# Optimization experiments

Hardware: AMD Instinct MI355X
Metric: run time of the kernel (lower is better)

The kernel has to match this reference:

```python
import jax, jax.numpy as jnp
import numpy as np

V, E, HID, NLAYERS, NL, B, T = 21128, 512, 512, 2, 9, 64, 512
H = HID // 2  # per-direction hidden


def setup_inputs() -> dict:
    key = jax.random.key(0)
    ks = jax.random.split(key, 12)
    n = lambda k, sh, sc=0.05: (jax.random.normal(k, sh, dtype=jnp.float32) * sc)
    return {
        "input_ids": jax.random.randint(ks[0], (B, T), 0, V),
        "labels": jax.random.randint(ks[1], (B, T), 0, NL),
        "emb": n(ks[2], (V, E), 0.02),
        # stacked LSTM params: [layer, direction, ...]; layer0 input = E == HID
        "w_ih": n(ks[3], (NLAYERS, 2, 4 * H, HID)),
        "w_hh": n(ks[4], (NLAYERS, 2, 4 * H, H)),
        "b_ih": n(ks[5], (NLAYERS, 2, 4 * H)),
        "b_hh": n(ks[6], (NLAYERS, 2, 4 * H)),
        "cls_w": n(ks[7], (NL, HID)),
        "cls_b": n(ks[8], (NL,)),
        "start_trans": jax.random.uniform(ks[9], (NL,), jnp.float32, -0.1, 0.1),
        "end_trans": jax.random.uniform(ks[10], (NL,), jnp.float32, -0.1, 0.1),
        "trans": jax.random.uniform(ks[11], (NL, NL), jnp.float32, -0.1, 0.1),
    }


def _lstm_dir(x, wi, wh, bi, bh, reverse):
    # x: [B,T,I] -> h: [B,T,H]; torch gate order i,f,g,o
    xp = jnp.einsum('bti,gi->btg', x, wi) + bi + bh  # [B,T,4H]
    if reverse:
        xp = xp[:, ::-1]
    h0 = jnp.zeros((x.shape[0], wh.shape[1]), x.dtype)

    def step(carry, xt):
        h, c = carry
        g = xt + h @ wh.T
        i, f, gg, o = jnp.split(g, 4, axis=-1)
        c = jax.nn.sigmoid(f) * c + jax.nn.sigmoid(i) * jnp.tanh(gg)
        h = jax.nn.sigmoid(o) * jnp.tanh(c)
        return (h, c), h

    _, hs = jax.lax.scan(step, (h0, h0), xp.swapaxes(0, 1))
    hs = hs.swapaxes(0, 1)
    return hs[:, ::-1] if reverse else hs


def _crf_neg_llh(logits, labels, start_trans, end_trans, trans):
    # torchcrf forward, full mask, reduction='sum'; returns -sum(log-likelihood)
    em0 = logits[:, 0]  # [B,NL]
    alpha0 = start_trans[None, :] + em0
    num0 = start_trans[labels[:, 0]] + jnp.take_along_axis(em0, labels[:, 0:1], 1)[:, 0]

    def step(carry, xt):
        alpha, num, prev = carry
        em, tag = xt  # [B,NL], [B]
        alpha = jax.nn.logsumexp(alpha[:, :, None] + trans[None] + em[:, None, :], axis=1)
        num = num + trans[prev, tag] + jnp.take_along_axis(em, tag[:, None], 1)[:, 0]
        return (alpha, num, tag), None

    xs = (logits[:, 1:].swapaxes(0, 1), labels[:, 1:].swapaxes(0, 1))
    (alpha, num, last), _ = jax.lax.scan(step, (alpha0, num0, labels[:, 0]), xs)
    denom = jax.nn.logsumexp(alpha + end_trans[None, :], axis=1)
    num = num + end_trans[last]
    return -jnp.sum(num - denom)


def reference(input_ids, labels, emb, w_ih, w_hh, b_ih, b_hh, cls_w, cls_b,
              start_trans, end_trans, trans):
    x = emb[input_ids]  # [B,T,E]
    for l in range(NLAYERS):
        fwd = _lstm_dir(x, w_ih[l, 0], w_hh[l, 0], b_ih[l, 0], b_hh[l, 0], False)
        bwd = _lstm_dir(x, w_ih[l, 1], w_hh[l, 1], b_ih[l, 1], b_hh[l, 1], True)
        x = jnp.concatenate([fwd, bwd], axis=-1)  # [B,T,HID]
    logits = jnp.einsum('bth,lh->btl', x, cls_w) + cls_b  # [B,T,NL]
    return _crf_neg_llh(logits, labels, start_trans, end_trans, trans)
```

## Files before the change

### kernel.cpp

```cpp
#include <hip/hip_runtime.h>

#define B_   64
#define T_   512
#define HID_ 512
#define H_   256
#define G4   1024
#define N2   2048
#define M_   (B_*T_)
#define NL_  9

typedef short short8 __attribute__((ext_vector_type(8)));
typedef float f32x4 __attribute__((ext_vector_type(4)));
typedef _Float16 f16x2 __attribute__((ext_vector_type(2)));

__device__ inline float bf2f(unsigned short u) {
  unsigned int x = ((unsigned int)u) << 16;
  return __builtin_bit_cast(float, x);
}
__device__ inline unsigned short f2bf(float f) {
  unsigned int u = __builtin_bit_cast(unsigned int, f);
  return (unsigned short)((u + 0x7fffu + ((u >> 16) & 1u)) >> 16);
}
__device__ inline unsigned short f2h(float f) {
  _Float16 h = (_Float16)f;
  return __builtin_bit_cast(unsigned short, h);
}
__device__ inline float fdot2(unsigned int w, unsigned int h, float acc) {
#if __has_builtin(__builtin_amdgcn_fdot2)
  return __builtin_amdgcn_fdot2(__builtin_bit_cast(f16x2, w),
                                __builtin_bit_cast(f16x2, h), acc, false);
#else
  f16x2 a = __builtin_bit_cast(f16x2, w), b = __builtin_bit_cast(f16x2, h);
  return acc + (float)a[0]*(float)b[0] + (float)a[1]*(float)b[1];
#endif
}
__device__ inline float sigm(float x)     { return 1.f / (1.f + __expf(-x)); }
__device__ inline float tanhfast(float x) { return 1.f - 2.f / (__expf(2.f*x) + 1.f); }

__device__ inline float xhalf_sum(float x) {
#if __has_builtin(__builtin_amdgcn_permlane32_swap)
  typedef unsigned int u32x2 __attribute__((ext_vector_type(2)));
  u32x2 r = __builtin_amdgcn_permlane32_swap(
      __builtin_bit_cast(unsigned int, x), __builtin_bit_cast(unsigned int, x),
      false, false);
  return x + __builtin_bit_cast(float, r[1]);
#else
  return x + __shfl_xor(x, 32, 64);
#endif
}

__device__ inline void gload16(const unsigned short* g, unsigned short* l) {
  __builtin_amdgcn_global_load_lds(
      (const __attribute__((address_space(1))) void*)g,
      (__attribute__((address_space(3))) void*)l, 16, 0, 0);
}

__global__ void k_cast_bf16(const float* __restrict__ src, unsigned short* __restrict__ dst, int n) {
  int i = blockIdx.x*256 + threadIdx.x;
  if (i < n) dst[i] = f2bf(src[i]);
}

__global__ void k_pack_whh(const float* __restrict__ whh, unsigned int* __restrict__ wr,
                           unsigned int* __restrict__ wl) {
  int idx = blockIdx.x*256 + threadIdx.x;
  int q   = idx & 3;
  int t   = (idx >> 2) & 511;
  int i4  = (idx >> 11) & 63;
  int ld  = idx >> 17;
  int lane = t & 63, wave = t >> 6;
  int u  = wave*32 + (lane & 31);
  int kh = lane >> 5;
  int g, k0;
  if (i4 < 48) { g = i4/12; int j = i4%12; k0 = kh*128 + 8*j + 2*q; }
  else         { int m = i4-48; g = m>>2; int jl = m&3; k0 = kh*128 + 96 + 8*jl + 2*q; }
  int c = g*256 + u;
  const float* src = whh + ((size_t)ld*1024 + c)*256 + k0;
  unsigned int pack = (unsigned int)f2h(src[0]) | ((unsigned int)f2h(src[1]) << 16);
  if (i4 < 48) wr[(((size_t)ld*48 + i4)*512 + t)*4 + q] = pack;
  else         wl[(((size_t)ld*16 + (i4-48))*512 + t)*4 + q] = pack;
}

__global__ void k_bias_sum(const float* __restrict__ bi, const float* __restrict__ bh,
                           float* __restrict__ bs) {
  int i = blockIdx.x*256 + threadIdx.x;
  if (i < 4096) bs[i] = bi[i] + bh[i];
}

__global__ void k_cls_pad(const float* __restrict__ w, unsigned short* __restrict__ dst) {
  int i = blockIdx.x*256 + threadIdx.x;
  if (i < 16*512) {
    int n = i >> 9, k = i & 511;
    dst[i] = (n < NL_) ? f2bf(w[n*512 + k]) : (unsigned short)0;
  }
}

__global__ void k_embed(const int* __restrict__ ids, const float* __restrict__ emb,
                        unsigned short* __restrict__ x0) {
  int idx = blockIdx.x*256 + threadIdx.x;
  int m  = idx >> 7;
  int e4 = (idx & 127) << 2;
  int id = ids[m];
  float4 v = *(const float4*)(emb + (size_t)id*HID_ + e4);
  unsigned short* dst = x0 + (size_t)m*HID_ + e4;
  dst[0]=f2bf(v.x); dst[1]=f2bf(v.y); dst[2]=f2bf(v.z); dst[3]=f2bf(v.w);
}

__global__ __launch_bounds__(256) void k_gemm_inproj(const unsigned short* __restrict__ A,
    const unsigned short* __restrict__ Bt, const float* __restrict__ bias,
    unsigned short* __restrict__ C) {
  __shared__ unsigned short As[4096];
  __shared__ unsigned short Bs[4096];
  int tid  = threadIdx.x;
  int lane = tid & 63, w = tid >> 6;
  int wm = w >> 1, wn = w & 1;
  int n0 = blockIdx.x * 128;
  int m0 = blockIdx.y * 128;

  int c0 = tid, c1 = 256 + tid;
  int ar0 = c0 & 127, ak0 = c0 >> 7;
  int ar1 = c1 & 127, ak1 = c1 >> 7;
  const unsigned short* gA0 = A  + (size_t)(m0 + ar0)*512 + ak0*8;
  const unsigned short* gA1 = A  + (size_t)(m0 + ar1)*512 + ak1*8;
  const unsigned short* gB0 = Bt + (size_t)(n0 + ar0)*512 + ak0*8;
  const unsigned short* gB1 = Bt + (size_t)(n0 + ar1)*512 + ak1*8;
  unsigned short* lA0 = As + (size_t)c0*8;
  unsigned short* lA1 = As + (size_t)c1*8;
  unsigned short* lB0 = Bs + (size_t)c0*8;
  unsigned short* lB1 = Bs + (size_t)c1*8;

  int r = lane & 15, kg = lane >> 4;
  const short8* Af = (const short8*)As + (size_t)kg*128 + wm*64 + r;
  const short8* Bf = (const short8*)Bs + (size_t)kg*128 + wn*64 + r;

  f32x4 acc[4][4];
  #pragma unroll
  for (int mi = 0; mi < 4; mi++)
    #pragma unroll
    for (int ni = 0; ni < 4; ni++)
      acc[mi][ni] = (f32x4){0,0,0,0};

  #pragma unroll 1
  for (int kt = 0; kt < 16; kt++) {
    gload16(gA0, lA0); gload16(gA1, lA1);
    gload16(gB0, lB0); gload16(gB1, lB1);
    gA0 += 32; gA1 += 32; gB0 += 32; gB1 += 32;
    __syncthreads();
    short8 av[4], bv[4];
    #pragma unroll
    for (int i = 0; i < 4; i++) { av[i] = Af[i*16]; bv[i] = Bf[i*16]; }
    #pragma unroll
    for (int mi = 0; mi < 4; mi++)
      #pragma unroll
      for (int ni = 0; ni < 4; ni++)
        acc[mi][ni] = __builtin_amdgcn_mfma_f32_16x16x32_bf16(av[mi], bv[ni], acc[mi][ni], 0, 0, 0);
    __syncthreads();
  }

  int rbase = m0 + wm*64 + (lane >> 4)*4;
  int cbase = n0 + wn*64 + (lane & 15);
  #pragma unroll
  for (int ni = 0; ni < 4; ni++) {
    int n = cbase + ni*16;
    float bb = bias[n];
    int dd = n >> 10, nn = n & 1023, uu = nn & 255, gg = nn >> 8;
    size_t ncol = (size_t)dd*1024 + uu*4 + gg;
    #pragma unroll
    for (int mi = 0; mi < 4; mi++)
      #pragma unroll
      for (int rr = 0; rr < 4; rr++)
        C[(size_t)(rbase + mi*16 + rr)*N2 + ncol] = f2bf(acc[mi][ni][rr] + bb);
  }
}

__global__ __launch_bounds__(256) void k_cls(const unsigned short* __restrict__ X,
    const unsigned short* __restrict__ Wb, const float* __restrict__ cb,
    float* __restrict__ out) {
  int lane = threadIdx.x & 63, wave = threadIdx.x >> 6;
  int m0 = blockIdx.x*64 + wave*16;
  int r = lane & 15, kg = lane >> 4;
  const short8* Ap = (const short8*)(X  + (size_t)(m0 + r)*512 + kg*8);
  const short8* Bp = (const short8*)(Wb + (size_t)r*512 + kg*8);
  f32x4 acc = {0,0,0,0};
  #pragma unroll
  for (int kb = 0; kb < 16; kb++)
    acc = __builtin_amdgcn_mfma_f32_16x16x32_bf16(Ap[kb*4], Bp[kb*4], acc, 0, 0, 0);
  int row0 = m0 + (lane >> 4)*4, col = lane & 15;
  if (col < NL_) {
    float bb = cb[col];
    #pragma unroll
    for (int rr = 0; rr < 4; rr++)
      out[(size_t)(row0+rr)*NL_ + col] = acc[rr] + bb;
  }
}

#define DOT4(ACC, W0, W1, W2, W3, HH) do { \
  ACC = fdot2(W0, (HH).x, ACC); ACC = fdot2(W1, (HH).y, ACC); \
  ACC = fdot2(W2, (HH).z, ACC); ACC = fdot2(W3, (HH).w, ACC); } while(0)

__global__ __launch_bounds__(512, 2) void k_rec(const unsigned short* __restrict__ xp,
    const uint4* __restrict__ wr, const uint4* __restrict__ wl,
    unsigned short* __restrict__ xout, int layer) {
  extern __shared__ char smem[];
  unsigned int* hA = (unsigned int*)(smem + 131072);
  unsigned int* hB = hA + 128;
  int t = threadIdx.x;
  int lane = t & 63, wave = t >> 6;
  int u  = wave*32 + (lane & 31);
  int kh = lane >> 5;
  bool lo = (lane < 32);
  int b = blockIdx.x >> 1, d = blockIdx.x & 1;
  int ld = layer*2 + d;

  char* wlb = smem + (((unsigned)(t*16)) ^ (((unsigned)t & 0x38u) << 1));
  {
    const uint4* src = wl + (size_t)ld*16*512 + t;
    #pragma unroll
    for (int m = 0; m < 16; m++)
      *(uint4*)(wlb + m*8192) = src[(size_t)m*512];
  }
  uint4 wq[48];
  {
    const uint4* src = wr + (size_t)ld*48*512 + t;
    #pragma unroll
    for (int i = 0; i < 48; i++) wq[i] = src[(size_t)i*512];
  }
  if (t < 128) hA[t] = 0u;
  float cst = 0.f;
  const unsigned short* xbase = xp + (size_t)b*T_*N2 + (size_t)d*G4 + u*4;
  unsigned short* obase = xout + (size_t)b*T_*HID_ + d*H_ + u;
  __syncthreads();

  int tt = d ? (T_-1) : 0;
  ushort4 nx = {0,0,0,0};
  if (lo) nx = *(const ushort4*)(xbase + (size_t)tt*N2);
  #pragma unroll 1
  for (int step = 0; step < T_; step++) {
    const uint4* hs = (const uint4*)((step & 1) ? hB : hA) + kh*16;
    float a0 = bf2f(nx.x), a1 = bf2f(nx.y), a2 = bf2f(nx.z), a3 = bf2f(nx.w);
    int ttn = d ? (T_-2-step) : (step+1);
    if (lo && step < T_-1)
      nx = *(const ushort4*)(xbase + (size_t)ttn*N2);
    #pragma unroll
    for (int j = 0; j < 12; j++) {
      uint4 hh = hs[j];
      DOT4(a0, wq[j].x,    wq[j].y,    wq[j].z,    wq[j].w,    hh);
      DOT4(a1, wq[12+j].x, wq[12+j].y, wq[12+j].z, wq[12+j].w, hh);
      DOT4(a2, wq[24+j].x, wq[24+j].y, wq[24+j].z, wq[24+j].w, hh);
      DOT4(a3, wq[36+j].x, wq[36+j].y, wq[36+j].z, wq[36+j].w, hh);
    }
    #pragma unroll
    for (int jl = 0; jl < 4; jl++) {
      uint4 hh = hs[12 + jl];
      uint4 q0 = *(const uint4*)(wlb + (0*4+jl)*8192);
      uint4 q1 = *(const uint4*)(wlb + (1*4+jl)*8192);
      uint4 q2 = *(const uint4*)(wlb + (2*4+jl)*8192);
      uint4 q3 = *(const uint4*)(wlb + (3*4+jl)*8192);
      DOT4(a0, q0.x, q0.y, q0.z, q0.w, hh);
      DOT4(a1, q1.x, q1.y, q1.z, q1.w, hh);
      DOT4(a2, q2.x, q2.y, q2.z, q2.w, hh);
      DOT4(a3, q3.x, q3.y, q3.z, q3.w, hh);
    }
    a0 = xhalf_sum(a0); a1 = xhalf_sum(a1);
    a2 = xhalf_sum(a2); a3 = xhalf_sum(a3);
    if (lo) {
      float gi = sigm(a0);
      float gf = sigm(a1);
      float gg = tanhfast(a2);
      float go = sigm(a3);
      cst = gf*cst + gi*gg;
      float h = go * tanhfast(cst);
      _Float16* hn = (_Float16*)((step & 1) ? hA : hB);
      hn[u] = (_Float16)h;
      obase[(size_t)tt*HID_] = f2bf(h);
    }
    __syncthreads();
    tt = ttn;
  }
}

__global__ void k_zero(float* out) { if (threadIdx.x == 0) out[0] = 0.f; }

__global__ void k_crf(const float* __restrict__ logits, const int* __restrict__ labels,
                      const float* __restrict__ st, const float* __restrict__ et,
                      const float* __restrict__ tr, float* __restrict__ out) {
  int b = blockIdx.x, lane = threadIdx.x;
  bool act = lane < NL_;
  const float* lb = logits + (size_t)b*T_*NL_;
  float trc[9];
  #pragma unroll
  for (int i = 0; i < 9; i++) trc[i] = act ? tr[i*9 + lane] : 0.f;
  float em = act ? lb[lane] : -1e30f;
  float alpha = act ? (st[lane] + em) : -1e30f;
  int prev = labels[b*T_];
  float num = __shfl(alpha, prev);
  for (int ttt = 1; ttt < T_; ttt++) {
    em = act ? lb[ttt*NL_ + lane] : -1e30f;
    float vv[9]; float mx = -1e30f;
    #pragma unroll
    for (int i = 0; i < 9; i++) { vv[i] = __shfl(alpha, i) + trc[i]; mx = fmaxf(mx, vv[i]); }
    float s = 0.f;
    #pragma unroll
    for (int i = 0; i < 9; i++) s += __expf(vv[i] - mx);
    alpha = act ? (mx + __logf(s) + em) : -1e30f;
    int tag = labels[b*T_ + ttt];
    float emtag = __shfl(em, tag);
    if (lane == 0) num += tr[prev*9 + tag] + emtag;
    prev = tag;
  }
  float fa = act ? (alpha + et[lane]) : -1e30f;
  float mx = -1e30f;
  #pragma unroll
  for (int i = 0; i < 9; i++) mx = fmaxf(mx, __shfl(fa, i));
  float s = 0.f;
  #pragma unroll
  for (int i = 0; i < 9; i++) s += __expf(__shfl(fa, i) - mx);
  float denom = mx + __logf(s);
  if (lane == 0) {
    num += et[prev];
    atomicAdd(out, denom - num);
  }
}

extern "C" void kernel_launch(void* const* d_in, const int* in_sizes, int n_in,
                              void* d_out, int out_size, void* d_ws, size_t ws_size,
                              hipStream_t stream) {
  const int*   ids    = (const int*)d_in[0];
  const int*   labels = (const int*)d_in[1];
  const float* emb    = (const float*)d_in[2];
  const float* w_ih   = (const float*)d_in[3];
  const float* w_hh   = (const float*)d_in[4];
  const float* b_ih   = (const float*)d_in[5];
  const float* b_hh   = (const float*)d_in[6];
  const float* cls_w  = (const float*)d_in[7];
  const float* cls_b  = (const float*)d_in[8];
  const float* st     = (const float*)d_in[9];
  const float* et     = (const float*)d_in[10];
  const float* tr     = (const float*)d_in[11];
  float* out = (float*)d_out;

  char* ws = (char*)d_ws;
  unsigned short* xp    = (unsigned short*)(ws);
  unsigned short* x0    = (unsigned short*)(ws + 134217728);
  unsigned short* x1    = (unsigned short*)(ws + 167772160);
  unsigned short* wbi   = (unsigned short*)(ws + 201326592);
  unsigned int*   wreg  = (unsigned int*)  (ws + 205520896);
  unsigned int*   wldsg = (unsigned int*)  (ws + 207093760);
  float*          bsum  = (float*)         (ws + 207618048);
  unsigned short* clswb = (unsigned short*)(ws + 207634432);
  float*          logit = (float*)         (ws + 207650816);

  const int REC_SMEM = 131072 + 1024;
  hipFuncSetAttribute((const void*)k_rec, hipFuncAttributeMaxDynamicSharedMemorySize, REC_SMEM);

  k_cast_bf16<<<8192, 256, 0, stream>>>(w_ih, wbi, 2*N2*512);
  k_pack_whh <<<2048, 256, 0, stream>>>(w_hh, wreg, wldsg);
  k_bias_sum <<<16,   256, 0, stream>>>(b_ih, b_hh, bsum);
  k_cls_pad  <<<32,   256, 0, stream>>>(cls_w, clswb);
  k_embed    <<<16384,256, 0, stream>>>(ids, emb, x0);

  dim3 ggrid(16, 256);
  k_gemm_inproj<<<ggrid, 256, 0, stream>>>(x0, wbi, bsum, xp);
  k_rec<<<128, 512, REC_SMEM, stream>>>(xp, (const uint4*)wreg, (const uint4*)wldsg, x1, 0);
  k_gemm_inproj<<<ggrid, 256, 0, stream>>>(x1, wbi + (size_t)N2*512, bsum + 2048, xp);
  k_rec<<<128, 512, REC_SMEM, stream>>>(xp, (const uint4*)wreg, (const uint4*)wldsg, x0, 1);
  k_cls<<<512, 256, 0, stream>>>(x0, clswb, cls_b, logit);
  k_zero<<<1, 64, 0, stream>>>(out);
  k_crf<<<64, 64, 0, stream>>>(logit, labels, st, et, tr, out);
}
```

Baseline: 2.464 ms.

## Remap input-projection GEMM tiles to emit gate-interleaved vectorized stores

The input-projection GEMM now assigns each block 32 hidden units across all four gates of one direction. Each thread therefore holds the i,f,g,o values for one unit and writes them as a single ushort4 into the interleaved xp layout, replacing scattered 2-byte stores. The bias is pre-permuted to match, and the weight cast and embedding kernels use vector loads and stores. In the recurrence, the per-step input load becomes unconditional with a clamped index and a lane select, which removes divergent branches at the cost of redundant loads.

```diff
diff --git a/kernel.cpp b/kernel.cpp
--- a/kernel.cpp
+++ b/kernel.cpp
@@ -55,9 +55,14 @@
       (__attribute__((address_space(3))) void*)l, 16, 0, 0);
 }
 
-__global__ void k_cast_bf16(const float* __restrict__ src, unsigned short* __restrict__ dst, int n) {
+__global__ void k_cast_bf16x4(const float4* __restrict__ src, ushort4* __restrict__ dst, int n4) {
   int i = blockIdx.x*256 + threadIdx.x;
-  if (i < n) dst[i] = f2bf(src[i]);
+  if (i < n4) {
+    float4 v = src[i];
+    ushort4 o;
+    o.x = f2bf(v.x); o.y = f2bf(v.y); o.z = f2bf(v.z); o.w = f2bf(v.w);
+    dst[i] = o;
+  }
 }
 
 __global__ void k_pack_whh(const float* __restrict__ whh, unsigned int* __restrict__ wr,
@@ -83,7 +88,11 @@
 __global__ void k_bias_sum(const float* __restrict__ bi, const float* __restrict__ bh,
                            float* __restrict__ bs) {
   int i = blockIdx.x*256 + threadIdx.x;
-  if (i < 4096) bs[i] = bi[i] + bh[i];
+  if (i < 4096) {
+    int l = i >> 11, r = i & 2047;
+    int dd = r >> 10, nn = r & 1023, g = nn >> 8, u = nn & 255;
+    bs[l*2048 + dd*1024 + u*4 + g] = bi[i] + bh[i];
+  }
 }
 
 __global__ void k_cls_pad(const float* __restrict__ w, unsigned short* __restrict__ dst) {
@@ -101,8 +110,9 @@
   int e4 = (idx & 127) << 2;
   int id = ids[m];
   float4 v = *(const float4*)(emb + (size_t)id*HID_ + e4);
-  unsigned short* dst = x0 + (size_t)m*HID_ + e4;
-  dst[0]=f2bf(v.x); dst[1]=f2bf(v.y); dst[2]=f2bf(v.z); dst[3]=f2bf(v.w);
+  ushort4 o;
+  o.x = f2bf(v.x); o.y = f2bf(v.y); o.z = f2bf(v.z); o.w = f2bf(v.w);
+  *(ushort4*)(x0 + (size_t)m*HID_ + e4) = o;
 }
 
 __global__ __launch_bounds__(256) void k_gemm_inproj(const unsigned short* __restrict__ A,
@@ -113,16 +123,19 @@
   int tid  = threadIdx.x;
   int lane = tid & 63, w = tid >> 6;
   int wm = w >> 1, wn = w & 1;
-  int n0 = blockIdx.x * 128;
+  int d  = blockIdx.x >> 3;
+  int u0 = (blockIdx.x & 7) * 32;
   int m0 = blockIdx.y * 128;
 
   int c0 = tid, c1 = 256 + tid;
   int ar0 = c0 & 127, ak0 = c0 >> 7;
   int ar1 = c1 & 127, ak1 = c1 >> 7;
+  int br0 = d*1024 + (ar0 >> 5)*256 + u0 + (ar0 & 31);
+  int br1 = d*1024 + (ar1 >> 5)*256 + u0 + (ar1 & 31);
   const unsigned short* gA0 = A  + (size_t)(m0 + ar0)*512 + ak0*8;
   const unsigned short* gA1 = A  + (size_t)(m0 + ar1)*512 + ak1*8;
-  const unsigned short* gB0 = Bt + (size_t)(n0 + ar0)*512 + ak0*8;
-  const unsigned short* gB1 = Bt + (size_t)(n0 + ar1)*512 + ak1*8;
+  const unsigned short* gB0 = Bt + (size_t)br0*512 + ak0*8;
+  const unsigned short* gB1 = Bt + (size_t)br1*512 + ak1*8;
   unsigned short* lA0 = As + (size_t)c0*8;
   unsigned short* lA1 = As + (size_t)c1*8;
   unsigned short* lB0 = Bs + (size_t)c0*8;
@@ -130,7 +143,7 @@
 
   int r = lane & 15, kg = lane >> 4;
   const short8* Af = (const short8*)As + (size_t)kg*128 + wm*64 + r;
-  const short8* Bf = (const short8*)Bs + (size_t)kg*128 + wn*64 + r;
+  const short8* Bf = (const short8*)Bs + (size_t)kg*128 + wn*16 + r;
 
   f32x4 acc[4][4];
   #pragma unroll
@@ -147,7 +160,7 @@
     __syncthreads();
     short8 av[4], bv[4];
     #pragma unroll
-    for (int i = 0; i < 4; i++) { av[i] = Af[i*16]; bv[i] = Bf[i*16]; }
+    for (int i = 0; i < 4; i++) { av[i] = Af[i*16]; bv[i] = Bf[i*32]; }
     #pragma unroll
     for (int mi = 0; mi < 4; mi++)
       #pragma unroll
@@ -157,19 +170,19 @@
   }
 
   int rbase = m0 + wm*64 + (lane >> 4)*4;
-  int cbase = n0 + wn*64 + (lane & 15);
-  #pragma unroll
-  for (int ni = 0; ni < 4; ni++) {
-    int n = cbase + ni*16;
-    float bb = bias[n];
-    int dd = n >> 10, nn = n & 1023, uu = nn & 255, gg = nn >> 8;
-    size_t ncol = (size_t)dd*1024 + uu*4 + gg;
-    #pragma unroll
-    for (int mi = 0; mi < 4; mi++)
-      #pragma unroll
-      for (int rr = 0; rr < 4; rr++)
-        C[(size_t)(rbase + mi*16 + rr)*N2 + ncol] = f2bf(acc[mi][ni][rr] + bb);
-  }
+  int ucol  = u0 + wn*16 + (lane & 15);
+  float4 bb = *(const float4*)(bias + (size_t)d*1024 + ucol*4);
+  #pragma unroll
+  for (int mi = 0; mi < 4; mi++)
+    #pragma unroll
+    for (int rr = 0; rr < 4; rr++) {
+      ushort4 o;
+      o.x = f2bf(acc[mi][0][rr] + bb.x);
+      o.y = f2bf(acc[mi][1][rr] + bb.y);
+      o.z = f2bf(acc[mi][2][rr] + bb.z);
+      o.w = f2bf(acc[mi][3][rr] + bb.w);
+      *(ushort4*)(C + (size_t)(rbase + mi*16 + rr)*N2 + d*1024 + ucol*4) = o;
+    }
 }
 
 __global__ __launch_bounds__(256) void k_cls(const unsigned short* __restrict__ X,
@@ -231,15 +244,18 @@
   __syncthreads();
 
   int tt = d ? (T_-1) : 0;
-  ushort4 nx = {0,0,0,0};
-  if (lo) nx = *(const ushort4*)(xbase + (size_t)tt*N2);
+  ushort4 nx = *(const ushort4*)(xbase + (size_t)tt*N2);
   #pragma unroll 1
   for (int step = 0; step < T_; step++) {
+    int ttn = d ? (T_-2-step) : (step+1);
+    int ttc = (step < T_-1) ? ttn : tt;
+    ushort4 cx = nx;
+    nx = *(const ushort4*)(xbase + (size_t)ttc*N2);
     const uint4* hs = (const uint4*)((step & 1) ? hB : hA) + kh*16;
-    float a0 = bf2f(nx.x), a1 = bf2f(nx.y), a2 = bf2f(nx.z), a3 = bf2f(nx.w);
-    int ttn = d ? (T_-2-step) : (step+1);
-    if (lo && step < T_-1)
-      nx = *(const ushort4*)(xbase + (size_t)ttn*N2);
+    float a0 = lo ? bf2f(cx.x) : 0.f;
+    float a1 = lo ? bf2f(cx.y) : 0.f;
+    float a2 = lo ? bf2f(cx.z) : 0.f;
+    float a3 = lo ? bf2f(cx.w) : 0.f;
     #pragma unroll
     for (int j = 0; j < 12; j++) {
       uint4 hh = hs[j];
@@ -352,7 +368,7 @@
   const int REC_SMEM = 131072 + 1024;
   hipFuncSetAttribute((const void*)k_rec, hipFuncAttributeMaxDynamicSharedMemorySize, REC_SMEM);
 
-  k_cast_bf16<<<8192, 256, 0, stream>>>(w_ih, wbi, 2*N2*512);
+  k_cast_bf16x4<<<2048, 256, 0, stream>>>((const float4*)w_ih, (ushort4*)wbi, 2*N2*512/4);
   k_pack_whh <<<2048, 256, 0, stream>>>(w_hh, wreg, wldsg);
   k_bias_sum <<<16,   256, 0, stream>>>(b_ih, b_hh, bsum);
   k_cls_pad  <<<32,   256, 0, stream>>>(cls_w, clswb);
```

After: 2.361 ms. 1.04x faster.
